# Performance work log

Hardware: AMD Instinct MI355X
Metric: run time of the kernel (lower is better)

Reference implementation:

```python
import jax, jax.numpy as jnp
import numpy as np

T, H, I, E, SI, TOP_K = 1024, 2048, 1408, 60, 5632, 4


def setup_inputs() -> dict:
    key = jax.random.key(0)
    ks = jax.random.split(key, 9)
    s = 0.02  # typical init scale for weights
    return {
        "x": jax.random.normal(ks[0], (T, H), jnp.float32),
        "router_w": jax.random.normal(ks[1], (E, H), jnp.float32) * s,
        "w_gate": jax.random.normal(ks[2], (E, I, H), jnp.float32) * s,
        "w_up": jax.random.normal(ks[3], (E, I, H), jnp.float32) * s,
        "w_down": jax.random.normal(ks[4], (E, H, I), jnp.float32) * s,
        "sw_gate": jax.random.normal(ks[5], (SI, H), jnp.float32) * s,
        "sw_up": jax.random.normal(ks[6], (SI, H), jnp.float32) * s,
        "sw_down": jax.random.normal(ks[7], (H, SI), jnp.float32) * s,
        "shared_gate_w": jax.random.normal(ks[8], (1, H), jnp.float32) * s,
        "top_k": TOP_K,
    }


def reference(x, router_w, w_gate, w_up, w_down, sw_gate, sw_up, sw_down, shared_gate_w, top_k):
    Ttok, Hdim = x.shape
    Eexp = router_w.shape[0]
    # --- router: softmax over experts, top-k selection (norm_topk_prob=False) ---
    logits = x @ router_w.T                          # [T,E]
    probs = jax.nn.softmax(logits, axis=-1)
    topk_p, topk_i = jax.lax.top_k(probs, top_k)     # [T,k]
    # dense combine weights: zero for unrouted experts
    combine = jnp.zeros((Ttok, Eexp), x.dtype)
    combine = combine.at[jnp.arange(Ttok)[:, None], topk_i].set(topk_p)  # [T,E]

    # --- routed experts: SwiGLU MLP per expert, weighted accumulate (scan over E) ---
    def expert_step(acc, w):
        wg, wu, wd, c = w                            # [I,H],[I,H],[H,I],[T]
        h = jax.nn.silu(x @ wg.T) * (x @ wu.T)       # [T,I]
        return acc + c[:, None] * (h @ wd.T), None

    moe_out, _ = jax.lax.scan(expert_step, jnp.zeros_like(x),
                              (w_gate, w_up, w_down, combine.T))

    # --- shared expert with sigmoid gate ---
    shared = (jax.nn.silu(x @ sw_gate.T) * (x @ sw_up.T)) @ sw_down.T    # [T,H]
    shared = jax.nn.sigmoid(x @ shared_gate_w.T) * shared                # [T,1]*[T,H]
    return moe_out + shared
```

## Files before the change

kernel.cpp:

```cpp
#include <hip/hip_runtime.h>
#include <hip/hip_bf16.h>


typedef float  f32x4  __attribute__((ext_vector_type(4)));
typedef short  bf16x8 __attribute__((ext_vector_type(8)));
typedef unsigned short u16;
typedef unsigned int   u32;

constexpr int TT = 1024, HD = 2048, ID = 1408, NE = 60, SID = 5632, KTOP = 4;
constexpr int NBR_GU = (ID / 128) * NE;
constexpr int NB_GU  = NBR_GU + (SID / 128) * (TT / 128);
constexpr int NBS_DN = (HD / 64) * (TT / 128);
constexpr int NB_DN  = NBS_DN + (HD / 64) * NE;

#define GLDS(g, l) __builtin_amdgcn_global_load_lds( \
    (const __attribute__((address_space(1))) void*)(g), \
    (__attribute__((address_space(3))) void*)(l), 16, 0, 0)
#define GL4(dst, ptr) asm volatile("global_load_dwordx4 %0, %1, off" : "=&v"(dst) : "v"(ptr))
#define WAITVM(n) do { asm volatile("s_waitcnt vmcnt(" #n ")" ::: "memory"); \
                       __builtin_amdgcn_sched_barrier(0); } while (0)
#define LGKMBAR() do { asm volatile("s_waitcnt lgkmcnt(0)" ::: "memory"); \
    __builtin_amdgcn_s_barrier(); \
    asm volatile("" ::: "memory"); } while (0)

__device__ __forceinline__ u16 f2bf(float f) {
    union { float f; u32 u; } v; v.f = f;
    u32 r = v.u + 0x7FFFu + ((v.u >> 16) & 1u);
    return (u16)(r >> 16);
}
__device__ __forceinline__ u32 cvtpk(float a, float b) {
    u32 r; asm("v_cvt_pk_bf16_f32 %0, %1, %2" : "=v"(r) : "v"(a), "v"(b));
    return r;
}
__device__ __forceinline__ bf16x8 cvt8(f32x4 a, f32x4 b) {
    union { u32 u[4]; bf16x8 v; } rr;
    rr.u[0] = cvtpk(a[0], a[1]); rr.u[1] = cvtpk(a[2], a[3]);
    rr.u[2] = cvtpk(b[0], b[1]); rr.u[3] = cvtpk(b[2], b[3]);
    return rr.v;
}

__global__ void zero_k(int* __restrict__ p) { p[threadIdx.x] = 0; }

__global__ __launch_bounds__(256) void zeroout_k(float* __restrict__ p) {
    ((float4*)p)[blockIdx.x * 256 + threadIdx.x] = make_float4(0.f, 0.f, 0.f, 0.f);
}

__global__ __launch_bounds__(256) void xcvt_k(const float* __restrict__ x, u16* __restrict__ xb)
{
    size_t i = ((size_t)blockIdx.x * 256 + threadIdx.x) * 16;
    const float4* p = (const float4*)(x + i);
    float4 f0 = p[0], f1 = p[1], f2 = p[2], f3 = p[3];
    uint4 o0, o1;
    o0.x = cvtpk(f0.x, f0.y); o0.y = cvtpk(f0.z, f0.w);
    o0.z = cvtpk(f1.x, f1.y); o0.w = cvtpk(f1.z, f1.w);
    o1.x = cvtpk(f2.x, f2.y); o1.y = cvtpk(f2.z, f2.w);
    o1.z = cvtpk(f3.x, f3.y); o1.w = cvtpk(f3.z, f3.w);
    ((uint4*)(xb + i))[0] = o0;
    ((uint4*)(xb + i))[1] = o1;
}

__global__ __launch_bounds__(64) void router_k(
    const float* __restrict__ x, const float* __restrict__ rw,
    const float* __restrict__ sgw,
    float* __restrict__ topk_p, int* __restrict__ topk_i,
    int* __restrict__ cnt, float* __restrict__ sgate)
{
    const int t = blockIdx.x, l = threadIdx.x;
    const float4* xr = ((const float4*)(x + (size_t)t * HD)) + l * 8;
    float4 xa[8];
    #pragma unroll
    for (int i = 0; i < 8; i++) xa[i] = xr[i];

    float le = 0.f;
    for (int e = 0; e < NE; e++) {
        const float4* wr = ((const float4*)(rw + (size_t)e * HD)) + l * 8;
        float a = 0.f;
        #pragma unroll
        for (int i = 0; i < 8; i++) {
            float4 wv = wr[i];
            a += xa[i].x * wv.x + xa[i].y * wv.y + xa[i].z * wv.z + xa[i].w * wv.w;
        }
        #pragma unroll
        for (int s = 32; s; s >>= 1) a += __shfl_xor(a, s);
        if (l == e) le = a;
    }
    {
        const float4* wr = ((const float4*)sgw) + l * 8;
        float a = 0.f;
        #pragma unroll
        for (int i = 0; i < 8; i++) {
            float4 wv = wr[i];
            a += xa[i].x * wv.x + xa[i].y * wv.y + xa[i].z * wv.z + xa[i].w * wv.w;
        }
        #pragma unroll
        for (int s = 32; s; s >>= 1) a += __shfl_xor(a, s);
        if (l == 0) sgate[t] = 1.f / (1.f + __expf(-a));
    }
    float mv = (l < NE) ? le : -3.4e38f;
    #pragma unroll
    for (int s = 32; s; s >>= 1) mv = fmaxf(mv, __shfl_xor(mv, s));
    float p = (l < NE) ? __expf(le - mv) : 0.f;
    float ss = p;
    #pragma unroll
    for (int s = 32; s; s >>= 1) ss += __shfl_xor(ss, s);
    p /= ss;
    float pv = (l < NE) ? p : -1.f;
    int   pi = l;
    float kp = 0.f; int ki = 0;
    for (int k = 0; k < KTOP; k++) {
        float bv = pv; int bi = pi;
        #pragma unroll
        for (int s = 32; s; s >>= 1) {
            float ov = __shfl_xor(bv, s); int oi = __shfl_xor(bi, s);
            if (ov > bv || (ov == bv && oi < bi)) { bv = ov; bi = oi; }
        }
        if (l == k) { kp = bv; ki = bi; }
        if (pi == bi) pv = -1.f;
    }
    if (l < KTOP) {
        topk_p[t * KTOP + l] = kp;
        topk_i[t * KTOP + l] = ki;
        atomicAdd(&cnt[ki], 1);
    }
}

__global__ __launch_bounds__(64) void prefix_k(const int* __restrict__ cnt, int* __restrict__ base)
{
    int l = threadIdx.x;
    if (l < NE) {
        int s = 0;
        for (int j = 0; j < l; j++) s += cnt[j];
        base[l] = s;
    }
}

__global__ __launch_bounds__(256) void scatter_k(
    const float* __restrict__ topk_p, const int* __restrict__ topk_i,
    const int* __restrict__ base, int* __restrict__ fill,
    int* __restrict__ slot_tok, float* __restrict__ slot_wt)
{
    int t = blockIdx.x * blockDim.x + threadIdx.x;
    if (t >= TT) return;
    for (int k = 0; k < KTOP; k++) {
        int e = topk_i[t * KTOP + k];
        int pos = atomicAdd(&fill[e], 1);
        int s = base[e] + pos;
        slot_tok[s] = t;
        slot_wt[s]  = topk_p[t * KTOP + k];
    }
}

__global__ __launch_bounds__(512, 2) void gu_all(
    const u16* __restrict__ Xb,
    const float* __restrict__ w_gate, const float* __restrict__ w_up,
    const float* __restrict__ sw_g, const float* __restrict__ sw_u,
    u16* __restrict__ h, u16* __restrict__ hs,
    const int* __restrict__ slot_tok, const float* __restrict__ slot_wt,
    const int* __restrict__ cnt, const int* __restrict__ basea)
{
    __shared__ u16 Asl[4][128 * 32];
    __shared__ u16 Bgsl[2][128 * 32];
    __shared__ u16 Busl[2][128 * 32];

    const int bid = blockIdx.x;
    const bool grouped = bid < NBR_GU;
    const int tid = threadIdx.x, w = tid >> 6, lane = tid & 63;
    const int lm = lane & 15, lk = lane >> 4;
    const int wm0 = (w >> 2) * 64, wn0 = (w & 3) * 32;

    int e = 0, my = 0, nb;
    const float *Wg, *Wu; u16* Hout; int Nout;
    if (grouped) {
        e = bid / 11; nb = bid % 11;
        Wg = w_gate + (size_t)e * ID * HD; Wu = w_up + (size_t)e * ID * HD;
        Hout = h; Nout = ID;
    } else {
        int sid = bid - NBR_GU; my = sid / 44; nb = sid % 44;
        Wg = sw_g; Wu = sw_u; Hout = hs; Nout = SID;
    }
    const int mcnt  = grouped ? cnt[e] : 128;
    const int mbase = grouped ? basea[e] : 0;

    const int ars = tid >> 2;
    const int aCh = (((tid & 3) ^ (ars & 3) ^ ((ars >> 2) & 3))) << 3;
    const int segA = (w * 16) * 32;
    const int brt = tid >> 2, bkc = tid & 3;
    const float* pg = Wg + (size_t)(nb * 128 + brt) * HD + bkc * 8;
    const float* pu = Wu + (size_t)(nb * 128 + brt) * HD + bkc * 8;
    const int bWr = brt * 32 + ((bkc ^ ((brt >> 1) & 3)) << 3);

    int aOff[4], bOff[2];
    #pragma unroll
    for (int mf = 0; mf < 4; mf++) {
        int r = wm0 + mf * 16 + lm;
        aOff[mf] = r * 32 + ((lk ^ (r & 3) ^ ((r >> 2) & 3)) << 3);
    }
    #pragma unroll
    for (int nf = 0; nf < 2; nf++) {
        int rb = wn0 + nf * 16 + lm;
        bOff[nf] = rb * 32 + ((lk ^ ((rb >> 1) & 3)) << 3);
    }
    const int nk = HD >> 5;

    for (int mt = 0; grouped ? (mt * 128 < mcnt) : (mt == 0); ++mt) {
        const u16* aSrc;
        {
            int row;
            if (grouped) {
                int sl = mbase + mt * 128 + ars;
                row = (mt * 128 + ars < mcnt) ? slot_tok[sl] : slot_tok[mbase];
            } else row = my * 128 + ars;
            aSrc = Xb + (size_t)row * HD + aCh;
        }

        f32x4 accG[4][2], accU[4][2];
        #pragma unroll
        for (int mf = 0; mf < 4; mf++)
            #pragma unroll
            for (int nf = 0; nf < 2; nf++) {
                accG[mf][nf] = f32x4{0.f, 0.f, 0.f, 0.f};
                accU[mf][nf] = f32x4{0.f, 0.f, 0.f, 0.f};
            }

        f32x4 ga0, ga1, ua0, ua1;
        f32x4 gb0, gb1, ub0, ub1;

#define ISSUE(G0_, G1_, U0_, U1_, AB, KT) do {                                \
        GL4(G0_, pg + (KT)); GL4(G1_, pg + (KT) + 4);                         \
        GL4(U0_, pu + (KT)); GL4(U1_, pu + (KT) + 4);                         \
        GLDS(aSrc + (KT), &Asl[AB][segA]);                                    \
    } while (0)

#define WRITEB(G0_, G1_, U0_, U1_, BB) do {                                   \
        *(bf16x8*)&Bgsl[BB][bWr] = cvt8(G0_, G1_);                            \
        *(bf16x8*)&Busl[BB][bWr] = cvt8(U0_, U1_);                            \
    } while (0)

#define COMPSTEP(AB, BB) do {                                                 \
        bf16x8 af[4], bg[2], bu_[2];                                          \
        _Pragma("unroll")                                                     \
        for (int mf = 0; mf < 4; mf++) af[mf] = *(const bf16x8*)&Asl[AB][aOff[mf]]; \
        _Pragma("unroll")                                                     \
        for (int nf = 0; nf < 2; nf++) {                                      \
            bg[nf]  = *(const bf16x8*)&Bgsl[BB][bOff[nf]];                    \
            bu_[nf] = *(const bf16x8*)&Busl[BB][bOff[nf]];                    \
        }                                                                     \
        _Pragma("unroll")                                                     \
        for (int mf = 0; mf < 4; mf++)                                        \
            _Pragma("unroll")                                                 \
            for (int nf = 0; nf < 2; nf++) {                                  \
                accG[mf][nf] = __builtin_amdgcn_mfma_f32_16x16x32_bf16(af[mf], bg[nf],  accG[mf][nf], 0, 0, 0); \
                accU[mf][nf] = __builtin_amdgcn_mfma_f32_16x16x32_bf16(af[mf], bu_[nf], accU[mf][nf], 0, 0, 0); \
            }                                                                 \
    } while (0)

        ISSUE(ga0, ga1, ua0, ua1, 0, 0);
        ISSUE(gb0, gb1, ub0, ub1, 1, 32);
        WAITVM(5);
        WRITEB(ga0, ga1, ua0, ua1, 0);
        LGKMBAR();

        for (int t = 0; t < nk; t += 4) {
            if (t + 2 < nk) { ISSUE(ga0, ga1, ua0, ua1, 2, (t + 2) << 5); COMPSTEP(0, 0); WAITVM(5); }
            else            { COMPSTEP(0, 0); WAITVM(0); }
            if (t + 1 < nk) WRITEB(gb0, gb1, ub0, ub1, 1);
            LGKMBAR();
            if (t + 3 < nk) { ISSUE(gb0, gb1, ub0, ub1, 3, (t + 3) << 5); COMPSTEP(1, 1); WAITVM(5); }
            else            { COMPSTEP(1, 1); WAITVM(0); }
            if (t + 2 < nk) WRITEB(ga0, ga1, ua0, ua1, 0);
            LGKMBAR();
            if (t + 4 < nk) { ISSUE(ga0, ga1, ua0, ua1, 0, (t + 4) << 5); COMPSTEP(2, 0); WAITVM(5); }
            else            { COMPSTEP(2, 0); WAITVM(0); }
            if (t + 3 < nk) WRITEB(gb0, gb1, ub0, ub1, 1);
            LGKMBAR();
            if (t + 5 < nk) { ISSUE(gb0, gb1, ub0, ub1, 1, (t + 5) << 5); COMPSTEP(3, 1); WAITVM(5); }
            else            { COMPSTEP(3, 1); WAITVM(0); }
            if (t + 4 < nk) WRITEB(ga0, ga1, ua0, ua1, 0);
            LGKMBAR();
        }
#undef ISSUE
#undef WRITEB
#undef COMPSTEP

        #pragma unroll
        for (int mf = 0; mf < 4; mf++)
            #pragma unroll
            for (int j = 0; j < 4; j++) {
                int m = wm0 + mf * 16 + lk * 4 + j;
                bool valid = grouped ? (mt * 128 + m < mcnt) : true;
                if (valid) {
                    size_t row; float wt;
                    if (grouped) {
                        size_t sl = (size_t)(mbase + mt * 128 + m);
                        row = sl; wt = slot_wt[sl];
                    } else { row = (size_t)(my * 128 + m); wt = 1.f; }
                    #pragma unroll
                    for (int nf = 0; nf < 2; nf++) {
                        int col = nb * 128 + wn0 + nf * 16 + lm;
                        float g = accG[mf][nf][j], u = accU[mf][nf][j];
                        float hv = g / (1.f + __expf(-g)) * u * wt;
                        Hout[row * (size_t)Nout + col] = f2bf(hv);
                    }
                }
            }
    }
}

__global__ __launch_bounds__(256, 3) void down_all(
    const u16* __restrict__ h, const u16* __restrict__ hs,
    const float* __restrict__ w_down, const float* __restrict__ sw_d,
    float* __restrict__ outF,
    const int* __restrict__ slot_tok, const float* __restrict__ sgate,
    const int* __restrict__ cnt, const int* __restrict__ basea)
{
    __shared__ u16 Asl[4][128 * 32];
    __shared__ u16 Bsl[2][64 * 32];

    const int bid = blockIdx.x;
    const bool shared_m = bid < NBS_DN;
    const int tid = threadIdx.x, w = tid >> 6, lane = tid & 63;
    const int lm = lane & 15, lk = lane >> 4;
    const int wm0 = (w >> 1) * 64, wn0 = (w & 1) * 32;

    int e = 0, my = 0, nb, K;
    const u16* Ap; const float* Wp;
    if (shared_m) {
        my = bid / 32; nb = bid % 32; K = SID; Ap = hs; Wp = sw_d;
    } else {
        int rid = bid - NBS_DN; e = rid / 32; nb = rid % 32; K = ID;
        Ap = h; Wp = w_down + (size_t)e * HD * ID;
    }
    const int mcnt  = shared_m ? 128 : cnt[e];
    const int mbase = shared_m ? 0 : basea[e];

    const int aCh = (((lane & 3) ^ ((lane >> 2) & 3) ^ ((lane >> 4) & 3))) << 3;
    const int brow_s = tid >> 2, bkc = tid & 3;
    const float* pb = Wp + (size_t)(nb * 64 + brow_s) * K + bkc * 8;
    const int bWr = brow_s * 32 + ((bkc ^ ((brow_s >> 1) & 3)) << 3);

    int aOff[4], bOff[2];
    #pragma unroll
    for (int mf = 0; mf < 4; mf++) {
        int r = wm0 + mf * 16 + lm;
        aOff[mf] = r * 32 + ((lk ^ (r & 3) ^ ((r >> 2) & 3)) << 3);
    }
    #pragma unroll
    for (int nf = 0; nf < 2; nf++) {
        int rb = wn0 + nf * 16 + lm;
        bOff[nf] = rb * 32 + ((lk ^ ((rb >> 1) & 3)) << 3);
    }
    const int segA0 = (w * 32) * 32, segA1 = (w * 32 + 16) * 32;
    const int nk = K >> 5;

    for (int mt = 0; shared_m ? (mt == 0) : (mt * 128 < mcnt); ++mt) {
        const u16* aSrc0; const u16* aSrc1;
        {
            int m0 = w * 32 + (lane >> 2), m1 = m0 + 16;
            size_t r0, r1;
            if (shared_m) { r0 = (size_t)(my * 128 + m0); r1 = (size_t)(my * 128 + m1); }
            else { r0 = (size_t)(mbase + mt * 128 + m0); r1 = (size_t)(mbase + mt * 128 + m1); }
            aSrc0 = Ap + r0 * K + aCh;
            aSrc1 = Ap + r1 * K + aCh;
        }

        f32x4 acc[4][2];
        #pragma unroll
        for (int mf = 0; mf < 4; mf++)
            #pragma unroll
            for (int nf = 0; nf < 2; nf++) acc[mf][nf] = f32x4{0.f, 0.f, 0.f, 0.f};

        f32x4 ba0, ba1;
        f32x4 bb0, bb1;

#define ISSUE(B0_, B1_, AB, KT) do {                                          \
        GL4(B0_, pb + (KT)); GL4(B1_, pb + (KT) + 4);                         \
        GLDS(aSrc0 + (KT), &Asl[AB][segA0]);                                  \
        GLDS(aSrc1 + (KT), &Asl[AB][segA1]);                                  \
    } while (0)

#define WRITEB(B0_, B1_, BB) do {                                             \
        *(bf16x8*)&Bsl[BB][bWr] = cvt8(B0_, B1_);                             \
    } while (0)

#define COMPSTEP(AB, BB) do {                                                 \
        bf16x8 af[4], bf_[2];                                                 \
        _Pragma("unroll")                                                     \
        for (int mf = 0; mf < 4; mf++) af[mf] = *(const bf16x8*)&Asl[AB][aOff[mf]]; \
        _Pragma("unroll")                                                     \
        for (int nf = 0; nf < 2; nf++) bf_[nf] = *(const bf16x8*)&Bsl[BB][bOff[nf]]; \
        _Pragma("unroll")                                                     \
        for (int mf = 0; mf < 4; mf++)                                        \
            _Pragma("unroll")                                                 \
            for (int nf = 0; nf < 2; nf++)                                    \
                acc[mf][nf] = __builtin_amdgcn_mfma_f32_16x16x32_bf16(af[mf], bf_[nf], acc[mf][nf], 0, 0, 0); \
    } while (0)

        ISSUE(ba0, ba1, 0, 0);
        ISSUE(bb0, bb1, 1, 32);
        WAITVM(4);
        WRITEB(ba0, ba1, 0);
        LGKMBAR();

        for (int t = 0; t < nk; t += 4) {
            if (t + 2 < nk) { ISSUE(ba0, ba1, 2, (t + 2) << 5); COMPSTEP(0, 0); WAITVM(4); }
            else            { COMPSTEP(0, 0); WAITVM(0); }
            if (t + 1 < nk) WRITEB(bb0, bb1, 1);
            LGKMBAR();
            if (t + 3 < nk) { ISSUE(bb0, bb1, 3, (t + 3) << 5); COMPSTEP(1, 1); WAITVM(4); }
            else            { COMPSTEP(1, 1); WAITVM(0); }
            if (t + 2 < nk) WRITEB(ba0, ba1, 0);
            LGKMBAR();
            if (t + 4 < nk) { ISSUE(ba0, ba1, 0, (t + 4) << 5); COMPSTEP(2, 0); WAITVM(4); }
            else            { COMPSTEP(2, 0); WAITVM(0); }
            if (t + 3 < nk) WRITEB(bb0, bb1, 1);
            LGKMBAR();
            if (t + 5 < nk) { ISSUE(bb0, bb1, 1, (t + 5) << 5); COMPSTEP(3, 1); WAITVM(4); }
            else            { COMPSTEP(3, 1); WAITVM(0); }
            if (t + 4 < nk) WRITEB(ba0, ba1, 0);
            LGKMBAR();
        }
#undef ISSUE
#undef WRITEB
#undef COMPSTEP

        #pragma unroll
        for (int mf = 0; mf < 4; mf++)
            #pragma unroll
            for (int j = 0; j < 4; j++) {
                int m = wm0 + mf * 16 + lk * 4 + j;
                if (mt * 128 + m < mcnt) {
                    int tok; float scale;
                    if (shared_m) { tok = my * 128 + m; scale = sgate[tok]; }
                    else          { tok = slot_tok[mbase + mt * 128 + m]; scale = 1.f; }
                    #pragma unroll
                    for (int nf = 0; nf < 2; nf++) {
                        int col = nb * 64 + wn0 + nf * 16 + lm;
                        atomicAdd(&outF[(size_t)tok * HD + col], scale * acc[mf][nf][j]);
                    }
                }
            }
    }
}

extern "C" void kernel_launch(void* const* d_in, const int* in_sizes, int n_in,
                              void* d_out, int out_size, void* d_ws, size_t ws_size,
                              hipStream_t stream)
{
    const float* x      = (const float*)d_in[0];
    const float* rw     = (const float*)d_in[1];
    const float* w_gate = (const float*)d_in[2];
    const float* w_up   = (const float*)d_in[3];
    const float* w_down = (const float*)d_in[4];
    const float* sw_g   = (const float*)d_in[5];
    const float* sw_u   = (const float*)d_in[6];
    const float* sw_d   = (const float*)d_in[7];
    const float* sgw    = (const float*)d_in[8];
    float* out = (float*)d_out;

    char* ws = (char*)d_ws;
    int*   cnt      = (int*)(ws + 0);
    int*   fill     = (int*)(ws + 256);
    int*   basea    = (int*)(ws + 512);
    float* sgate    = (float*)(ws + 768);
    float* topk_p   = (float*)(ws + 5120);
    int*   topk_i   = (int*)(ws + 21504);
    int*   slot_tok = (int*)(ws + 37888);
    float* slot_wt  = (float*)(ws + 54272);
    u16*   xb = (u16*)(ws + 71680);
    u16*   h  = xb + (size_t)TT * HD;
    u16*   hs = h + (size_t)(4096 + 128) * ID;

    zero_k<<<1, 128, 0, stream>>>(cnt);
    zeroout_k<<<TT * HD / 1024, 256, 0, stream>>>(out);
    xcvt_k<<<512, 256, 0, stream>>>(x, xb);
    router_k<<<TT, 64, 0, stream>>>(x, rw, sgw, topk_p, topk_i, cnt, sgate);
    prefix_k<<<1, 64, 0, stream>>>(cnt, basea);
    scatter_k<<<4, 256, 0, stream>>>(topk_p, topk_i, basea, fill, slot_tok, slot_wt);

    gu_all<<<NB_GU, 512, 0, stream>>>(
        xb, w_gate, w_up, sw_g, sw_u, h, hs,
        slot_tok, slot_wt, cnt, basea);

    down_all<<<NB_DN, 256, 0, stream>>>(
        h, hs, w_down, sw_d, out,
        slot_tok, sgate, cnt, basea);
}
```

Before: 819.5 us.

## Replace down-proj atomics with slot buffer plus gather; async-load fp32 weights to LDS

The down-projection kernel no longer does float atomicAdd into the output. The shared-expert tiles store directly to the output, and the routed-expert tiles write bf16 per-slot results that a new gather kernel sums per token. This removes the zero-fill kernel and atomic contention. The B operand (fp32 weights) is now loaded straight into LDS with global_load_lds in a 3-stage ring and converted to bf16 at fragment-read time, replacing register staging with a manual conversion. The trade-offs are more LDS (fp32 B tiles), an extra launch, extra traffic for the slot buffer, and bf16 rounding of the per-expert partial outputs.

```diff
diff --git a/kernel.cpp b/kernel.cpp
--- a/kernel.cpp
+++ b/kernel.cpp
@@ -19,6 +19,9 @@
 #define GL4(dst, ptr) asm volatile("global_load_dwordx4 %0, %1, off" : "=&v"(dst) : "v"(ptr))
 #define WAITVM(n) do { asm volatile("s_waitcnt vmcnt(" #n ")" ::: "memory"); \
                        __builtin_amdgcn_sched_barrier(0); } while (0)
+#define BAR() do { asm volatile("" ::: "memory"); \
+    __builtin_amdgcn_s_barrier(); \
+    asm volatile("" ::: "memory"); } while (0)
 #define LGKMBAR() do { asm volatile("s_waitcnt lgkmcnt(0)" ::: "memory"); \
     __builtin_amdgcn_s_barrier(); \
     asm volatile("" ::: "memory"); } while (0)
@@ -27,6 +30,9 @@
     union { float f; u32 u; } v; v.f = f;
     u32 r = v.u + 0x7FFFu + ((v.u >> 16) & 1u);
     return (u16)(r >> 16);
+}
+__device__ __forceinline__ float bf2f(u16 b) {
+    union { float f; u32 u; } v; v.u = ((u32)b) << 16; return v.f;
 }
 __device__ __forceinline__ u32 cvtpk(float a, float b) {
     u32 r; asm("v_cvt_pk_bf16_f32 %0, %1, %2" : "=v"(r) : "v"(a), "v"(b));
@@ -40,10 +46,6 @@
 }
 
 __global__ void zero_k(int* __restrict__ p) { p[threadIdx.x] = 0; }
-
-__global__ __launch_bounds__(256) void zeroout_k(float* __restrict__ p) {
-    ((float4*)p)[blockIdx.x * 256 + threadIdx.x] = make_float4(0.f, 0.f, 0.f, 0.f);
-}
 
 __global__ __launch_bounds__(256) void xcvt_k(const float* __restrict__ x, u16* __restrict__ xb)
 {
@@ -59,6 +61,27 @@
     ((uint4*)(xb + i))[1] = o1;
 }
 
+__global__ __launch_bounds__(256) void gather_k(
+    const u16* __restrict__ dsl, const int* __restrict__ slot_of,
+    float* __restrict__ out)
+{
+    const int t = blockIdx.x;
+    const int c = threadIdx.x * 8;
+    const int s0 = slot_of[t * 4 + 0], s1 = slot_of[t * 4 + 1];
+    const int s2 = slot_of[t * 4 + 2], s3 = slot_of[t * 4 + 3];
+    bf16x8 v0 = *(const bf16x8*)&dsl[(size_t)s0 * HD + c];
+    bf16x8 v1 = *(const bf16x8*)&dsl[(size_t)s1 * HD + c];
+    bf16x8 v2 = *(const bf16x8*)&dsl[(size_t)s2 * HD + c];
+    bf16x8 v3 = *(const bf16x8*)&dsl[(size_t)s3 * HD + c];
+    float* op = out + (size_t)t * HD + c;
+    #pragma unroll
+    for (int i = 0; i < 8; i++) {
+        float s = bf2f((u16)v0[i]) + bf2f((u16)v1[i])
+                + bf2f((u16)v2[i]) + bf2f((u16)v3[i]);
+        op[i] += s;
+    }
+}
+
 __global__ __launch_bounds__(64) void router_k(
     const float* __restrict__ x, const float* __restrict__ rw,
     const float* __restrict__ sgw,
@@ -137,7 +160,8 @@
 __global__ __launch_bounds__(256) void scatter_k(
     const float* __restrict__ topk_p, const int* __restrict__ topk_i,
     const int* __restrict__ base, int* __restrict__ fill,
-    int* __restrict__ slot_tok, float* __restrict__ slot_wt)
+    int* __restrict__ slot_tok, float* __restrict__ slot_wt,
+    int* __restrict__ slot_of)
 {
     int t = blockIdx.x * blockDim.x + threadIdx.x;
     if (t >= TT) return;
@@ -147,6 +171,7 @@
         int s = base[e] + pos;
         slot_tok[s] = t;
         slot_wt[s]  = topk_p[t * KTOP + k];
+        slot_of[t * KTOP + k] = s;
     }
 }
 
@@ -309,12 +334,12 @@
 __global__ __launch_bounds__(256, 3) void down_all(
     const u16* __restrict__ h, const u16* __restrict__ hs,
     const float* __restrict__ w_down, const float* __restrict__ sw_d,
-    float* __restrict__ outF,
-    const int* __restrict__ slot_tok, const float* __restrict__ sgate,
+    float* __restrict__ outF, u16* __restrict__ dsl,
+    const float* __restrict__ sgate,
     const int* __restrict__ cnt, const int* __restrict__ basea)
 {
-    __shared__ u16 Asl[4][128 * 32];
-    __shared__ u16 Bsl[2][64 * 32];
+    __shared__ u16   Asl[3][128 * 32];
+    __shared__ float Bsl[3][64 * 32];
 
     const int bid = blockIdx.x;
     const bool shared_m = bid < NBS_DN;
@@ -334,11 +359,16 @@
     const int mbase = shared_m ? 0 : basea[e];
 
     const int aCh = (((lane & 3) ^ ((lane >> 2) & 3) ^ ((lane >> 4) & 3))) << 3;
-    const int brow_s = tid >> 2, bkc = tid & 3;
-    const float* pb = Wp + (size_t)(nb * 64 + brow_s) * K + bkc * 8;
-    const int bWr = brow_s * 32 + ((bkc ^ ((brow_s >> 1) & 3)) << 3);
-
-    int aOff[4], bOff[2];
+    const int bCh = ((lane & 7) ^ ((lane >> 3) & 7)) << 2;
+
+    const float* bSrc[2];
+    #pragma unroll
+    for (int j = 0; j < 2; j++) {
+        size_t rB = (size_t)(nb * 64 + w * 16 + j * 8 + (lane >> 3));
+        bSrc[j] = Wp + rB * K + bCh;
+    }
+
+    int aOff[4], bOff[2][2];
     #pragma unroll
     for (int mf = 0; mf < 4; mf++) {
         int r = wm0 + mf * 16 + lm;
@@ -347,20 +377,20 @@
     #pragma unroll
     for (int nf = 0; nf < 2; nf++) {
         int rb = wn0 + nf * 16 + lm;
-        bOff[nf] = rb * 32 + ((lk ^ ((rb >> 1) & 3)) << 3);
-    }
-    const int segA0 = (w * 32) * 32, segA1 = (w * 32 + 16) * 32;
+        bOff[nf][0] = rb * 32 + ((((lk << 1)    ) ^ (rb & 7)) << 2);
+        bOff[nf][1] = rb * 32 + ((((lk << 1) | 1) ^ (rb & 7)) << 2);
+    }
+
     const int nk = K >> 5;
 
     for (int mt = 0; shared_m ? (mt == 0) : (mt * 128 < mcnt); ++mt) {
-        const u16* aSrc0; const u16* aSrc1;
-        {
-            int m0 = w * 32 + (lane >> 2), m1 = m0 + 16;
-            size_t r0, r1;
-            if (shared_m) { r0 = (size_t)(my * 128 + m0); r1 = (size_t)(my * 128 + m1); }
-            else { r0 = (size_t)(mbase + mt * 128 + m0); r1 = (size_t)(mbase + mt * 128 + m1); }
-            aSrc0 = Ap + r0 * K + aCh;
-            aSrc1 = Ap + r1 * K + aCh;
+        const u16* aSrc[2];
+        #pragma unroll
+        for (int j = 0; j < 2; j++) {
+            int mrow = w * 32 + j * 16 + (lane >> 2);
+            size_t row = shared_m ? (size_t)(my * 128 + mrow)
+                                  : (size_t)(mbase + mt * 128 + mrow);
+            aSrc[j] = Ap + row * K + aCh;
         }
 
         f32x4 acc[4][2];
@@ -369,59 +399,41 @@
             #pragma unroll
             for (int nf = 0; nf < 2; nf++) acc[mf][nf] = f32x4{0.f, 0.f, 0.f, 0.f};
 
-        f32x4 ba0, ba1;
-        f32x4 bb0, bb1;
-
-#define ISSUE(B0_, B1_, AB, KT) do {                                          \
-        GL4(B0_, pb + (KT)); GL4(B1_, pb + (KT) + 4);                         \
-        GLDS(aSrc0 + (KT), &Asl[AB][segA0]);                                  \
-        GLDS(aSrc1 + (KT), &Asl[AB][segA1]);                                  \
-    } while (0)
-
-#define WRITEB(B0_, B1_, BB) do {                                             \
-        *(bf16x8*)&Bsl[BB][bWr] = cvt8(B0_, B1_);                             \
-    } while (0)
-
-#define COMPSTEP(AB, BB) do {                                                 \
-        bf16x8 af[4], bf_[2];                                                 \
-        _Pragma("unroll")                                                     \
-        for (int mf = 0; mf < 4; mf++) af[mf] = *(const bf16x8*)&Asl[AB][aOff[mf]]; \
-        _Pragma("unroll")                                                     \
-        for (int nf = 0; nf < 2; nf++) bf_[nf] = *(const bf16x8*)&Bsl[BB][bOff[nf]]; \
-        _Pragma("unroll")                                                     \
-        for (int mf = 0; mf < 4; mf++)                                        \
-            _Pragma("unroll")                                                 \
-            for (int nf = 0; nf < 2; nf++)                                    \
-                acc[mf][nf] = __builtin_amdgcn_mfma_f32_16x16x32_bf16(af[mf], bf_[nf], acc[mf][nf], 0, 0, 0); \
-    } while (0)
-
-        ISSUE(ba0, ba1, 0, 0);
-        ISSUE(bb0, bb1, 1, 32);
-        WAITVM(4);
-        WRITEB(ba0, ba1, 0);
-        LGKMBAR();
-
-        for (int t = 0; t < nk; t += 4) {
-            if (t + 2 < nk) { ISSUE(ba0, ba1, 2, (t + 2) << 5); COMPSTEP(0, 0); WAITVM(4); }
-            else            { COMPSTEP(0, 0); WAITVM(0); }
-            if (t + 1 < nk) WRITEB(bb0, bb1, 1);
-            LGKMBAR();
-            if (t + 3 < nk) { ISSUE(bb0, bb1, 3, (t + 3) << 5); COMPSTEP(1, 1); WAITVM(4); }
-            else            { COMPSTEP(1, 1); WAITVM(0); }
-            if (t + 2 < nk) WRITEB(ba0, ba1, 0);
-            LGKMBAR();
-            if (t + 4 < nk) { ISSUE(ba0, ba1, 0, (t + 4) << 5); COMPSTEP(2, 0); WAITVM(4); }
-            else            { COMPSTEP(2, 0); WAITVM(0); }
-            if (t + 3 < nk) WRITEB(bb0, bb1, 1);
-            LGKMBAR();
-            if (t + 5 < nk) { ISSUE(bb0, bb1, 1, (t + 5) << 5); COMPSTEP(3, 1); WAITVM(4); }
-            else            { COMPSTEP(3, 1); WAITVM(0); }
-            if (t + 4 < nk) WRITEB(ba0, ba1, 0);
-            LGKMBAR();
-        }
-#undef ISSUE
-#undef WRITEB
-#undef COMPSTEP
+        auto stage = [&](int b, int kt) {
+            #pragma unroll
+            for (int j = 0; j < 2; j++)
+                GLDS(aSrc[j] + kt, &Asl[b][(w * 32 + j * 16) * 32]);
+            #pragma unroll
+            for (int j = 0; j < 2; j++)
+                GLDS(bSrc[j] + kt, &Bsl[b][(w * 16 + j * 8) * 32]);
+        };
+        auto comp = [&](int b) {
+            const u16*   At = Asl[b];
+            const float* Bt = Bsl[b];
+            bf16x8 af[4];
+            #pragma unroll
+            for (int mf = 0; mf < 4; mf++) af[mf] = *(const bf16x8*)&At[aOff[mf]];
+            #pragma unroll
+            for (int nf = 0; nf < 2; nf++) {
+                bf16x8 bf_ = cvt8(*(const f32x4*)&Bt[bOff[nf][0]],
+                                  *(const f32x4*)&Bt[bOff[nf][1]]);
+                #pragma unroll
+                for (int mf = 0; mf < 4; mf++)
+                    acc[mf][nf] = __builtin_amdgcn_mfma_f32_16x16x32_bf16(af[mf], bf_, acc[mf][nf], 0, 0, 0);
+            }
+        };
+
+        stage(0, 0); stage(1, 32);
+        int t = 0, cb = 0;
+        for (; t + 2 < nk; ++t) {
+            int sbuf = cb - 1; if (sbuf < 0) sbuf += 3;
+            stage(sbuf, (t + 2) << 5);
+            WAITVM(8); BAR(); comp(cb); BAR();
+            cb = (cb + 1 == 3) ? 0 : cb + 1;
+        }
+        WAITVM(4); BAR(); comp(cb); BAR();
+        cb = (cb + 1 == 3) ? 0 : cb + 1;
+        WAITVM(0); BAR(); comp(cb); BAR();
 
         #pragma unroll
         for (int mf = 0; mf < 4; mf++)
@@ -429,13 +441,21 @@
             for (int j = 0; j < 4; j++) {
                 int m = wm0 + mf * 16 + lk * 4 + j;
                 if (mt * 128 + m < mcnt) {
-                    int tok; float scale;
-                    if (shared_m) { tok = my * 128 + m; scale = sgate[tok]; }
-                    else          { tok = slot_tok[mbase + mt * 128 + m]; scale = 1.f; }
-                    #pragma unroll
-                    for (int nf = 0; nf < 2; nf++) {
-                        int col = nb * 64 + wn0 + nf * 16 + lm;
-                        atomicAdd(&outF[(size_t)tok * HD + col], scale * acc[mf][nf][j]);
+                    if (shared_m) {
+                        int tok = my * 128 + m;
+                        float sc = sgate[tok];
+                        #pragma unroll
+                        for (int nf = 0; nf < 2; nf++) {
+                            int col = nb * 64 + wn0 + nf * 16 + lm;
+                            outF[(size_t)tok * HD + col] = sc * acc[mf][nf][j];
+                        }
+                    } else {
+                        size_t srow = (size_t)(mbase + mt * 128 + m);
+                        #pragma unroll
+                        for (int nf = 0; nf < 2; nf++) {
+                            int col = nb * 64 + wn0 + nf * 16 + lm;
+                            dsl[srow * HD + col] = f2bf(acc[mf][nf][j]);
+                        }
                     }
                 }
             }
@@ -469,19 +489,22 @@
     u16*   xb = (u16*)(ws + 71680);
     u16*   h  = xb + (size_t)TT * HD;
     u16*   hs = h + (size_t)(4096 + 128) * ID;
+    u16*   dsl = hs + (size_t)TT * SID;
+    int*   slot_of = (int*)(dsl + (size_t)(4096 + 128) * HD);
 
     zero_k<<<1, 128, 0, stream>>>(cnt);
-    zeroout_k<<<TT * HD / 1024, 256, 0, stream>>>(out);
     xcvt_k<<<512, 256, 0, stream>>>(x, xb);
     router_k<<<TT, 64, 0, stream>>>(x, rw, sgw, topk_p, topk_i, cnt, sgate);
     prefix_k<<<1, 64, 0, stream>>>(cnt, basea);
-    scatter_k<<<4, 256, 0, stream>>>(topk_p, topk_i, basea, fill, slot_tok, slot_wt);
+    scatter_k<<<4, 256, 0, stream>>>(topk_p, topk_i, basea, fill, slot_tok, slot_wt, slot_of);
 
     gu_all<<<NB_GU, 512, 0, stream>>>(
         xb, w_gate, w_up, sw_g, sw_u, h, hs,
         slot_tok, slot_wt, cnt, basea);
 
     down_all<<<NB_DN, 256, 0, stream>>>(
-        h, hs, w_down, sw_d, out,
-        slot_tok, sgate, cnt, basea);
-}
+        h, hs, w_down, sw_d, out, dsl,
+        sgate, cnt, basea);
+
+    gather_k<<<TT, 256, 0, stream>>>(dsl, slot_of, out);
+}
```

Measured after the change: 715.0 us. -12.8%, faster.
